# Optimization experiments

Measured on AMD Instinct MI355X. Metric: run time of the kernel, lower is better.

Reference implementation:

```python
import jax, jax.numpy as jnp
import numpy as np

N_WIRES = 4
DIM = 16  # 2**N_WIRES

# PauliZ eigenvalue signs per wire per basis state (wire 0 = MSB, torchquantum convention)
_Z = np.array([[1.0 - 2.0 * ((i >> (N_WIRES - 1 - w)) & 1) for i in range(DIM)]
               for w in range(N_WIRES)], dtype=np.float32)  # [4,16]

def _cnot_perm(c, t):
    mc = 1 << (N_WIRES - 1 - c)
    mt = 1 << (N_WIRES - 1 - t)
    return np.array([i ^ mt if (i & mc) else i for i in range(DIM)])

_PERM_WRAP = [_cnot_perm(0, 1), _cnot_perm(1, 2), _cnot_perm(2, 3), _cnot_perm(3, 0)]  # QLSTM ladder
_PERM_LINE = [_cnot_perm(0, 1), _cnot_perm(1, 2), _cnot_perm(2, 3)]                   # kernel ladder

def _apply_rx(state, theta, wire):
    """Apply RX(theta) on `wire`. state: [B,16] complex64. theta: scalar or [B]."""
    theta = jnp.asarray(theta)
    c = jnp.cos(theta / 2).astype(jnp.complex64)
    s = jnp.sin(theta / 2).astype(jnp.complex64)
    left = 2 ** wire
    right = 2 ** (N_WIRES - 1 - wire)
    st = state.reshape(-1, left, 2, right)
    a, b = st[:, :, 0, :], st[:, :, 1, :]
    if theta.ndim != 0:
        c = c[:, None, None]
        s = s[:, None, None]
    na = c * a - 1j * s * b
    nb = -1j * s * a + c * b
    return jnp.stack([na, nb], axis=2).reshape(-1, DIM)

def _circuit(angles, params, perms):
    """angles: [B,4] encoding RX angles; params: [4] trainable RX angles."""
    B = angles.shape[0]
    state = jnp.zeros((B, DIM), jnp.complex64).at[:, 0].set(1.0)
    for w in range(N_WIRES):
        state = _apply_rx(state, angles[:, w], w)
    for w in range(N_WIRES):
        state = _apply_rx(state, params[w], w)
    for p in perms:
        state = state[:, p]
    return state

def _measure_z(state):
    probs = state.real ** 2 + state.imag ** 2  # [B,16]
    return probs @ jnp.asarray(_Z).T           # [B,4]

def setup_inputs() -> dict:
    key = jax.random.key(0)
    ks = jax.random.split(key, 16)
    T, B, D, S, H = 128, 64, 32, 1024, 4
    inp = {
        'x': jax.random.normal(ks[0], (T, B, D), jnp.float32),
        'support_vectors': jax.random.normal(ks[1], (S, D), jnp.float32),
        'Wf': jax.random.normal(ks[2], (H, D + H), jnp.float32) * 0.1,
        'bf': jax.random.normal(ks[3], (H,), jnp.float32) * 0.1,
        'Wi': jax.random.normal(ks[4], (H, D + H), jnp.float32) * 0.1,
        'bi': jax.random.normal(ks[5], (H,), jnp.float32) * 0.1,
        'Wu': jax.random.normal(ks[6], (H, D + H), jnp.float32) * 0.1,
        'bu': jax.random.normal(ks[7], (H,), jnp.float32) * 0.1,
        'Wo': jax.random.normal(ks[8], (H, D + H), jnp.float32) * 0.1,
        'bo': jax.random.normal(ks[9], (H,), jnp.float32) * 0.1,
        'pf': jax.random.normal(ks[10], (H,), jnp.float32),
        'pi': jax.random.normal(ks[11], (H,), jnp.float32),
        'pu': jax.random.normal(ks[12], (H,), jnp.float32),
        'po': jax.random.normal(ks[13], (H,), jnp.float32),
        'qk_params': jax.random.normal(ks[14], (H,), jnp.float32),
    }
    return inp

def reference(x, support_vectors, Wf, bf, Wi, bi, Wu, bu, Wo, bo, pf, pi, pu, po, qk_params):
    T, B, D = x.shape
    gamma = 1.0
    xf = x.reshape(T * B, D)

    # classical RBF Gram matrix (materializes [N,S,D] diff, as in the original)
    diff = xf[:, None, :] - support_vectors[None, :, :]
    rbf = jnp.exp(-gamma * jnp.sum(diff * diff, axis=-1))  # [N,S]

    # quantum kernel: encode first 4 features, trainable RX, linear CNOT ladder
    sx = _circuit(xf[:, :4], qk_params, _PERM_LINE)               # [N,16] complex
    sy = _circuit(support_vectors[:, :4], qk_params, _PERM_LINE)  # [S,16] complex
    qk = jnp.abs(sx @ sy.T)  # no conjugation, matching torch.matmul(states_x, states_y.t())

    def gate(comb, W, b, p):
        return _measure_z(_circuit(comb @ W.T + b, p, _PERM_WRAP))

    def step(carry, xt):
        hx, cx = carry
        comb = jnp.concatenate([xt, hx], axis=1)
        f = jax.nn.sigmoid(gate(comb, Wf, bf, pf))
        i = jax.nn.sigmoid(gate(comb, Wi, bi, pi))
        g = jnp.tanh(gate(comb, Wu, bu, pu))
        o = jax.nn.sigmoid(gate(comb, Wo, bo, po))
        cx = f * cx + i * g
        hx = o * jnp.tanh(cx)
        return (hx, cx), hx

    h0 = jnp.zeros((B, N_WIRES), jnp.float32)
    c0 = jnp.zeros((B, N_WIRES), jnp.float32)
    (_, _), outs = jax.lax.scan(step, (h0, c0), x)  # outs: [T,B,4]
    return (outs, rbf, qk)
```

## Files before the change

### kernel.cpp

```cpp
#include <hip/hip_runtime.h>

#define T_STEPS 128
#define BATCH   64
#define DIMX    32
#define S_SUP   1024
#define NROW    8192
#define OUT_H_SZ   (T_STEPS*BATCH*4)
#define OUT_RBF_SZ (NROW*S_SUP)

#define INV2PI 0.15915494309189535f
#define L2E    1.4426950408889634f

__device__ __forceinline__ float rcp_fast(float x)  { return __builtin_amdgcn_rcpf(x); }
__device__ __forceinline__ float exp2_fast(float x) { return __builtin_amdgcn_exp2f(x); }
__device__ __forceinline__ float cos_rev(float x)   { return __builtin_amdgcn_cosf(x); }

template<int CTRL>
__device__ __forceinline__ float dpp_perm(float v) {
    return __builtin_bit_cast(float,
        __builtin_amdgcn_mov_dpp(__builtin_bit_cast(int, v), CTRL, 0xF, 0xF, true));
}
template<int K>
__device__ __forceinline__ float quad_bcast(float v) { return dpp_perm<K * 0x55>(v); }
#define DPP_XOR1 0xB1
#define DPP_XOR2 0x4E

__global__ __launch_bounds__(256) void pre_kernel(
    const float* __restrict__ x,
    const float* __restrict__ Wf, const float* __restrict__ bf,
    const float* __restrict__ Wi, const float* __restrict__ bi,
    const float* __restrict__ Wu, const float* __restrict__ bu,
    const float* __restrict__ Wo, const float* __restrict__ bo,
    const float* __restrict__ pf, const float* __restrict__ pi,
    const float* __restrict__ pu, const float* __restrict__ po,
    float* __restrict__ pre)
{
    const int tid = threadIdx.x;
    const int rl  = tid >> 4;
    const int gw  = tid & 15;
    const int g   = gw >> 2, w = gw & 3;
    const int row = blockIdx.x * 16 + rl;

    __shared__ float xs[16 * DIMX];
    if (tid < 128) {
        ((float4*)xs)[tid] = ((const float4*)(x + (size_t)blockIdx.x * 16 * DIMX))[tid];
    }
    __syncthreads();

    const float* W  = (g == 0) ? Wf : (g == 1) ? Wi : (g == 2) ? Wu : Wo;
    const float* bb = (g == 0) ? bf : (g == 1) ? bi : (g == 2) ? bu : bo;
    const float* pp = (g == 0) ? pf : (g == 1) ? pi : (g == 2) ? pu : po;

    float acc = bb[w] + pp[w];
    const float* Wr = W + w * 36;
    const float* xr = xs + rl * DIMX;
#pragma unroll
    for (int d = 0; d < DIMX; d++) acc += xr[d] * Wr[d];

    pre[(row * 4 + g) * 4 + w] = acc * INV2PI;
}

__global__ __launch_bounds__(512, 2) void fused_kernel(
    const float* __restrict__ x,  const float* __restrict__ sv,
    const float* __restrict__ Wf, const float* __restrict__ bf,
    const float* __restrict__ Wi, const float* __restrict__ bi,
    const float* __restrict__ Wu, const float* __restrict__ bu,
    const float* __restrict__ Wo, const float* __restrict__ bo,
    const float* __restrict__ pf, const float* __restrict__ pi,
    const float* __restrict__ pu, const float* __restrict__ po,
    const float* __restrict__ qkp, const float* __restrict__ pre,
    float* __restrict__ out_h, float* __restrict__ out_rbf, float* __restrict__ out_qk)
{
    __shared__ float xs[32 * DIMX];
    __shared__ float xn2[32];
    const int tid = threadIdx.x;

    if (blockIdx.x == 0) {
        if (tid >= 256) return;
        __builtin_amdgcn_s_setprio(3);
        const int b = tid >> 2, g = tid & 3;
        const float* W = (g == 0) ? Wf : (g == 1) ? Wi : (g == 2) ? Wu : Wo;

        float Wh[4][4];
#pragma unroll
        for (int w = 0; w < 4; w++)
#pragma unroll
            for (int j = 0; j < 4; j++) Wh[w][j] = W[w * 36 + 32 + j] * INV2PI;

        const float K2 = (g == 2) ? (-2.f * L2E) : (-L2E);
        const float Aa = (g == 2) ?  2.f :  1.f;
        const float Bb = (g == 2) ? -1.f :  0.f;
        const bool lb0 = (tid & 1) != 0;
        const bool lb1 = (tid & 2) != 0;

        float h = 0.f, c = 0.f;
        const int base = tid;
        const float4* prep = (const float4*)pre;

        auto lstm_step = [&](int t, float4 cur) {
            float hb0 = quad_bcast<0>(h);
            float hb1 = quad_bcast<1>(h);
            float hb2 = quad_bcast<2>(h);
            float hb3 = quad_bcast<3>(h);

            float a0 = cur.x + hb0 * Wh[0][0] + hb1 * Wh[0][1] + hb2 * Wh[0][2] + hb3 * Wh[0][3];
            float a1 = cur.y + hb0 * Wh[1][0] + hb1 * Wh[1][1] + hb2 * Wh[1][2] + hb3 * Wh[1][3];
            float a2 = cur.z + hb0 * Wh[2][0] + hb1 * Wh[2][1] + hb2 * Wh[2][2] + hb3 * Wh[2][3];
            float a3 = cur.w + hb0 * Wh[3][0] + hb1 * Wh[3][1] + hb2 * Wh[3][2] + hb3 * Wh[3][3];

            float C0 = cos_rev(a0), C1 = cos_rev(a1), C2 = cos_rev(a2), C3 = cos_rev(a3);
            float t23 = C2 * C3;
            float m01 = C0 * C1;
            float r0 = C1 * t23;
            float r1 = m01;
            float r2 = m01 * C2;
            float r3 = m01 * t23;

            float o0 = fmaf(Aa, rcp_fast(1.f + exp2_fast(r0 * K2)), Bb);
            float o1 = fmaf(Aa, rcp_fast(1.f + exp2_fast(r1 * K2)), Bb);
            float o2 = fmaf(Aa, rcp_fast(1.f + exp2_fast(r2 * K2)), Bb);
            float o3 = fmaf(Aa, rcp_fast(1.f + exp2_fast(r3 * K2)), Bb);

            float s0 = dpp_perm<DPP_XOR1>(o1);
            float s1 = dpp_perm<DPP_XOR1>(o0);
            float s2 = dpp_perm<DPP_XOR1>(o3);
            float s3 = dpp_perm<DPP_XOR1>(o2);
            float A0 = lb0 ? s0 : o0;
            float A1 = lb0 ? o1 : s1;
            float A2 = lb0 ? s2 : o2;
            float A3 = lb0 ? o3 : s3;
            float u0 = dpp_perm<DPP_XOR2>(A2);
            float u1 = dpp_perm<DPP_XOR2>(A3);
            float u2 = dpp_perm<DPP_XOR2>(A0);
            float u3 = dpp_perm<DPP_XOR2>(A1);
            float F = lb1 ? u0 : A0;
            float I = lb1 ? u1 : A1;
            float U = lb1 ? A2 : u2;
            float O = lb1 ? A3 : u3;

            c = fmaf(F, c, I * U);
            float e  = exp2_fast(c * (-2.f * L2E));
            float th = fmaf(2.f, rcp_fast(1.f + e), -1.f);
            h = O * th;

            out_h[t * 256 + tid] = h;
        };

        float4 cb0, cb1, cb2, cb3, cb4, cb5, cb6, cb7;
        cb0 = prep[base];           cb1 = prep[base + 256];
        cb2 = prep[base + 512];     cb3 = prep[base + 768];
        cb4 = prep[base + 1024];    cb5 = prep[base + 1280];
        cb6 = prep[base + 1536];    cb7 = prep[base + 1792];

#pragma unroll 1
        for (int tt = 0; tt < T_STEPS; tt += 8) {
            int nb = tt + 8; nb = (nb > T_STEPS - 8) ? (T_STEPS - 8) : nb;
            const float4* pc = prep + base + nb * 256;
            float4 nb0 = pc[0];
            float4 nb1 = pc[256];
            float4 nb2 = pc[512];
            float4 nb3 = pc[768];
            float4 nb4 = pc[1024];
            float4 nb5 = pc[1280];
            float4 nb6 = pc[1536];
            float4 nb7 = pc[1792];
            __builtin_amdgcn_sched_barrier(0);

            lstm_step(tt + 0, cb0);
            lstm_step(tt + 1, cb1);
            lstm_step(tt + 2, cb2);
            lstm_step(tt + 3, cb3);
            lstm_step(tt + 4, cb4);
            lstm_step(tt + 5, cb5);
            lstm_step(tt + 6, cb6);
            lstm_step(tt + 7, cb7);

            cb0 = nb0; cb1 = nb1; cb2 = nb2; cb3 = nb3;
            cb4 = nb4; cb5 = nb5; cb6 = nb6; cb7 = nb7;
        }
    } else {
        const int bid = blockIdx.x - 1;
        const int n0  = bid * 32;

        float4* xs4 = (float4*)xs;
        const float4* xg = (const float4*)(x + (size_t)n0 * DIMX);
        if (tid < 256) {
            float4 t0v = xg[tid];
            xs4[tid] = t0v;
            float p0 = t0v.x * t0v.x + t0v.y * t0v.y + t0v.z * t0v.z + t0v.w * t0v.w;
            p0 += __shfl_xor(p0, 1);
            p0 += __shfl_xor(p0, 2);
            p0 += __shfl_xor(p0, 4);
            if ((tid & 7) == 0) xn2[tid >> 3] = -L2E * p0;
        }

        const int sA = tid, sB = tid + 512;
        float4 svv[8], svw[8];
        const float4* svgA = (const float4*)(sv + (size_t)sA * DIMX);
        const float4* svgB = (const float4*)(sv + (size_t)sB * DIMX);
#pragma unroll
        for (int k = 0; k < 8; k++) { svv[k] = svgA[k]; svw[k] = svgB[k]; }
        float sn2A = 0.f, sn2B = 0.f;
#pragma unroll
        for (int k = 0; k < 8; k++) {
            sn2A += svv[k].x * svv[k].x + svv[k].y * svv[k].y + svv[k].z * svv[k].z + svv[k].w * svv[k].w;
            sn2B += svw[k].x * svw[k].x + svw[k].y * svw[k].y + svw[k].z * svw[k].z + svw[k].w * svw[k].w;
        }
        const float snlA = -L2E * sn2A;
        const float snlB = -L2E * sn2B;

        const float q0 = qkp[0], q1 = qkp[1], q2 = qkp[2], q3 = qkp[3];
        const float C05 = 0.5f * INV2PI;
        const float BA0 = fmaf(0.5f, svv[0].x, q0) * INV2PI;
        const float BA1 = fmaf(0.5f, svv[0].y, q1) * INV2PI;
        const float BA2 = fmaf(0.5f, svv[0].z, q2) * INV2PI;
        const float BA3 = fmaf(0.5f, svv[0].w, q3) * INV2PI;
        const float BB0 = fmaf(0.5f, svw[0].x, q0) * INV2PI;
        const float BB1 = fmaf(0.5f, svw[0].y, q1) * INV2PI;
        const float BB2 = fmaf(0.5f, svw[0].z, q2) * INV2PI;
        const float BB3 = fmaf(0.5f, svw[0].w, q3) * INV2PI;
        __syncthreads();

#pragma unroll 2
        for (int n = 0; n < 32; n++) {
            const float4* xr4 = (const float4*)(xs + n * DIMX);
            float4 xv0 = xr4[0];
            float dotA = xv0.x * svv[0].x + xv0.y * svv[0].y + xv0.z * svv[0].z + xv0.w * svv[0].w;
            float dotB = xv0.x * svw[0].x + xv0.y * svw[0].y + xv0.z * svw[0].z + xv0.w * svw[0].w;
#pragma unroll
            for (int k = 1; k < 8; k++) {
                float4 xv = xr4[k];
                dotA += xv.x * svv[k].x + xv.y * svv[k].y + xv.z * svv[k].z + xv.w * svv[k].w;
                dotB += xv.x * svw[k].x + xv.y * svw[k].y + xv.z * svw[k].z + xv.w * svw[k].w;
            }
            float xnl = xn2[n];
            float rbA = exp2_fast(fmaf(2.f * L2E, dotA, xnl + snlA));
            float rbB = exp2_fast(fmaf(2.f * L2E, dotB, xnl + snlB));

            float qvA = cos_rev(fmaf(C05, xv0.x, BA0)) * cos_rev(fmaf(C05, xv0.y, BA1))
                      * cos_rev(fmaf(C05, xv0.z, BA2)) * cos_rev(fmaf(C05, xv0.w, BA3));
            float qvB = cos_rev(fmaf(C05, xv0.x, BB0)) * cos_rev(fmaf(C05, xv0.y, BB1))
                      * cos_rev(fmaf(C05, xv0.z, BB2)) * cos_rev(fmaf(C05, xv0.w, BB3));
            qvA = fabsf(qvA);
            qvB = fabsf(qvB);

            const size_t rowb = (size_t)(n0 + n) * S_SUP;
            out_rbf[rowb + sA] = rbA;
            out_rbf[rowb + sB] = rbB;
            out_qk [rowb + sA] = qvA;
            out_qk [rowb + sB] = qvB;
        }
    }
}

extern "C" void kernel_launch(void* const* d_in, const int* in_sizes, int n_in,
                              void* d_out, int out_size, void* d_ws, size_t ws_size,
                              hipStream_t stream)
{
    const float* x   = (const float*)d_in[0];
    const float* sv  = (const float*)d_in[1];
    const float* Wf  = (const float*)d_in[2];
    const float* bf  = (const float*)d_in[3];
    const float* Wi  = (const float*)d_in[4];
    const float* bi  = (const float*)d_in[5];
    const float* Wu  = (const float*)d_in[6];
    const float* bu  = (const float*)d_in[7];
    const float* Wo  = (const float*)d_in[8];
    const float* bo  = (const float*)d_in[9];
    const float* pf  = (const float*)d_in[10];
    const float* pi  = (const float*)d_in[11];
    const float* pu  = (const float*)d_in[12];
    const float* po  = (const float*)d_in[13];
    const float* qkp = (const float*)d_in[14];

    float* out     = (float*)d_out;
    float* out_h   = out;
    float* out_rbf = out + OUT_H_SZ;
    float* out_qk  = out + OUT_H_SZ + OUT_RBF_SZ;

    float* pre = (float*)d_ws;

    pre_kernel<<<NROW / 16, 256, 0, stream>>>(x, Wf, bf, Wi, bi, Wu, bu, Wo, bo,
                                              pf, pi, pu, po, pre);
    fused_kernel<<<1 + 256, 512, 0, stream>>>(
        x, sv, Wf, bf, Wi, bi, Wu, bu, Wo, bo, pf, pi, pu, po, qkp, pre,
        out_h, out_rbf, out_qk);
}
```

Measured before the change: 134.9 us.

## Split LSTM recurrence across 512 threads with two wires per lane

The serial LSTM block now uses all 512 threads instead of 256. Each lane handles two of the four wires for one gate, which halves the per-lane cos/exp/rcp chain on the critical recurrence path. Cross-lane exchange moves from DPP quad broadcasts to ds_swizzle, and the tanh scaling is folded into the gate constants. The cost is extra swizzle traffic through the LDS crossbar, which has higher latency than DPP, and more waves competing with the RBF/QK blocks.

```diff
diff --git a/kernel.cpp b/kernel.cpp
--- a/kernel.cpp
+++ b/kernel.cpp
@@ -20,10 +20,13 @@
     return __builtin_bit_cast(float,
         __builtin_amdgcn_mov_dpp(__builtin_bit_cast(int, v), CTRL, 0xF, 0xF, true));
 }
-template<int K>
-__device__ __forceinline__ float quad_bcast(float v) { return dpp_perm<K * 0x55>(v); }
 #define DPP_XOR1 0xB1
-#define DPP_XOR2 0x4E
+
+template<int OFF>
+__device__ __forceinline__ float swz(float v) {
+    return __builtin_bit_cast(float,
+        __builtin_amdgcn_ds_swizzle(__builtin_bit_cast(int, v), OFF));
+}
 
 __global__ __launch_bounds__(256) void pre_kernel(
     const float* __restrict__ x,
@@ -76,94 +79,91 @@
     const int tid = threadIdx.x;
 
     if (blockIdx.x == 0) {
-        if (tid >= 256) return;
         __builtin_amdgcn_s_setprio(3);
-        const int b = tid >> 2, g = tid & 3;
+        const int lane = tid & 63;
+        const int wv   = tid >> 6;
+        const int g    = (lane >> 1) & 3;
+        const int wp   = lane & 1;
+        const bool iswp = wp != 0;
+        const bool hi2  = (lane & 4) != 0;
+        const int b     = wv * 8 + (lane >> 3);
+        const int wown  = 2 * wp + ((lane >> 2) & 1);
+        const int hbase = b * 4 + wown;
+
         const float* W = (g == 0) ? Wf : (g == 1) ? Wi : (g == 2) ? Wu : Wo;
-
-        float Wh[4][4];
-#pragma unroll
-        for (int w = 0; w < 4; w++)
-#pragma unroll
-            for (int j = 0; j < 4; j++) Wh[w][j] = W[w * 36 + 32 + j] * INV2PI;
+        float WhA[4], WhB[4];
+        const int wA = 2 * wp;
+#pragma unroll
+        for (int j = 0; j < 4; j++) {
+            WhA[j] = W[ wA      * 36 + 32 + j] * INV2PI;
+            WhB[j] = W[(wA + 1) * 36 + 32 + j] * INV2PI;
+        }
 
         const float K2 = (g == 2) ? (-2.f * L2E) : (-L2E);
-        const float Aa = (g == 2) ?  2.f :  1.f;
-        const float Bb = (g == 2) ? -1.f :  0.f;
-        const bool lb0 = (tid & 1) != 0;
-        const bool lb1 = (tid & 2) != 0;
-
-        float h = 0.f, c = 0.f;
-        const int base = tid;
-        const float4* prep = (const float4*)pre;
-
-        auto lstm_step = [&](int t, float4 cur) {
-            float hb0 = quad_bcast<0>(h);
-            float hb1 = quad_bcast<1>(h);
-            float hb2 = quad_bcast<2>(h);
-            float hb3 = quad_bcast<3>(h);
-
-            float a0 = cur.x + hb0 * Wh[0][0] + hb1 * Wh[0][1] + hb2 * Wh[0][2] + hb3 * Wh[0][3];
-            float a1 = cur.y + hb0 * Wh[1][0] + hb1 * Wh[1][1] + hb2 * Wh[1][2] + hb3 * Wh[1][3];
-            float a2 = cur.z + hb0 * Wh[2][0] + hb1 * Wh[2][1] + hb2 * Wh[2][2] + hb3 * Wh[2][3];
-            float a3 = cur.w + hb0 * Wh[3][0] + hb1 * Wh[3][1] + hb2 * Wh[3][2] + hb3 * Wh[3][3];
-
-            float C0 = cos_rev(a0), C1 = cos_rev(a1), C2 = cos_rev(a2), C3 = cos_rev(a3);
-            float t23 = C2 * C3;
-            float m01 = C0 * C1;
-            float r0 = C1 * t23;
-            float r1 = m01;
-            float r2 = m01 * C2;
-            float r3 = m01 * t23;
-
-            float o0 = fmaf(Aa, rcp_fast(1.f + exp2_fast(r0 * K2)), Bb);
-            float o1 = fmaf(Aa, rcp_fast(1.f + exp2_fast(r1 * K2)), Bb);
-            float o2 = fmaf(Aa, rcp_fast(1.f + exp2_fast(r2 * K2)), Bb);
-            float o3 = fmaf(Aa, rcp_fast(1.f + exp2_fast(r3 * K2)), Bb);
-
-            float s0 = dpp_perm<DPP_XOR1>(o1);
-            float s1 = dpp_perm<DPP_XOR1>(o0);
-            float s2 = dpp_perm<DPP_XOR1>(o3);
-            float s3 = dpp_perm<DPP_XOR1>(o2);
-            float A0 = lb0 ? s0 : o0;
-            float A1 = lb0 ? o1 : s1;
-            float A2 = lb0 ? s2 : o2;
-            float A3 = lb0 ? o3 : s3;
-            float u0 = dpp_perm<DPP_XOR2>(A2);
-            float u1 = dpp_perm<DPP_XOR2>(A3);
-            float u2 = dpp_perm<DPP_XOR2>(A0);
-            float u3 = dpp_perm<DPP_XOR2>(A1);
-            float F = lb1 ? u0 : A0;
-            float I = lb1 ? u1 : A1;
-            float U = lb1 ? A2 : u2;
-            float O = lb1 ? A3 : u3;
-
-            c = fmaf(F, c, I * U);
-            float e  = exp2_fast(c * (-2.f * L2E));
-            float th = fmaf(2.f, rcp_fast(1.f + e), -1.f);
+        const float Aa = (g == 2) ? (-4.f * L2E) : 1.f;
+        const float Bb = (g == 2) ? ( 2.f * L2E) : 0.f;
+
+        float h = 0.f, cs = 0.f;
+        const float2* prep2 = (const float2*)pre;
+
+        auto lstm_step = [&](int t, float2 cur) {
+            float h0 = swz<0x018>(h);
+            float h1 = swz<0x098>(h);
+            float h2 = swz<0x038>(h);
+            float h3 = swz<0x0B8>(h);
+
+            float aA = cur.x + h0 * WhA[0] + h1 * WhA[1] + h2 * WhA[2] + h3 * WhA[3];
+            float aB = cur.y + h0 * WhB[0] + h1 * WhB[1] + h2 * WhB[2] + h3 * WhB[3];
+            float CA = cos_rev(aA), CB = cos_rev(aB);
+
+            float DA = dpp_perm<DPP_XOR1>(CA);
+            float DB = dpp_perm<DPP_XOR1>(CB);
+
+            float P  = DA * DB;
+            float t1 = iswp ? CA : CB;
+            float rA = t1 * P;
+            float t2 = iswp ? rA : CA;
+            float rB = t2 * CB;
+
+            float sA = rcp_fast(1.f + exp2_fast(rA * K2));
+            float sB = rcp_fast(1.f + exp2_fast(rB * K2));
+            float oA = fmaf(Aa, sA, Bb);
+            float oB = fmaf(Aa, sB, Bb);
+
+            float FA = swz<0x019>(oA), FB = swz<0x019>(oB);
+            float IA = swz<0x059>(oA), IB = swz<0x059>(oB);
+            float UA = swz<0x099>(oA), UB = swz<0x099>(oB);
+            float OA = swz<0x0D9>(oA), OB = swz<0x0D9>(oB);
+            float F = hi2 ? FB : FA;
+            float I = hi2 ? IB : IA;
+            float U = hi2 ? UB : UA;
+            float O = hi2 ? OB : OA;
+
+            cs = fmaf(F, cs, I * U);
+            float th = fmaf(2.f, rcp_fast(1.f + exp2_fast(cs)), -1.f);
             h = O * th;
 
-            out_h[t * 256 + tid] = h;
+            out_h[t * 256 + hbase] = h;
         };
 
-        float4 cb0, cb1, cb2, cb3, cb4, cb5, cb6, cb7;
-        cb0 = prep[base];           cb1 = prep[base + 256];
-        cb2 = prep[base + 512];     cb3 = prep[base + 768];
-        cb4 = prep[base + 1024];    cb5 = prep[base + 1280];
-        cb6 = prep[base + 1536];    cb7 = prep[base + 1792];
+        float2 cb0, cb1, cb2, cb3, cb4, cb5, cb6, cb7;
+        cb0 = prep2[tid];            cb1 = prep2[tid + 512];
+        cb2 = prep2[tid + 1024];     cb3 = prep2[tid + 1536];
+        cb4 = prep2[tid + 2048];     cb5 = prep2[tid + 2560];
+        cb6 = prep2[tid + 3072];     cb7 = prep2[tid + 3584];
 
 #pragma unroll 1
         for (int tt = 0; tt < T_STEPS; tt += 8) {
             int nb = tt + 8; nb = (nb > T_STEPS - 8) ? (T_STEPS - 8) : nb;
-            const float4* pc = prep + base + nb * 256;
-            float4 nb0 = pc[0];
-            float4 nb1 = pc[256];
-            float4 nb2 = pc[512];
-            float4 nb3 = pc[768];
-            float4 nb4 = pc[1024];
-            float4 nb5 = pc[1280];
-            float4 nb6 = pc[1536];
-            float4 nb7 = pc[1792];
+            const float2* pc = prep2 + tid + nb * 512;
+            float2 nb0 = pc[0];
+            float2 nb1 = pc[512];
+            float2 nb2 = pc[1024];
+            float2 nb3 = pc[1536];
+            float2 nb4 = pc[2048];
+            float2 nb5 = pc[2560];
+            float2 nb6 = pc[3072];
+            float2 nb7 = pc[3584];
             __builtin_amdgcn_sched_barrier(0);
 
             lstm_step(tt + 0, cb0);
```

Result: no change. 132.8 us (-1.5%).
